# Kernel optimization log

Measured on AMD Instinct MI355X. Metric: run time of the kernel, lower is better.

The kernel has to match this reference:

```python
import jax, jax.numpy as jnp
from jax import lax
import numpy as np

NB_CODE = 16384
DIM = 128
SCALES = [(1, 1), (2, 2), (4, 4), (8, 8), (16, 16)]
PHI_IDX = [0, 1, 1, 2, 3]  # PhiPartiallyShared: argmin(|ticks - si/(SN-1)|), K=4, SN=5
RESI = 0.5  # abs(quant_resi)
BETA = 0.25


def _cubic(x, a=-0.75):
    # PyTorch bicubic kernel (cubic convolution, a=-0.75)
    ax = np.abs(x)
    return np.where(ax <= 1.0, (a + 2.0) * ax ** 3 - (a + 3.0) * ax ** 2 + 1.0,
                    np.where(ax < 2.0, a * ax ** 3 - 5.0 * a * ax ** 2 + 8.0 * a * ax - 4.0 * a, 0.0))


def bicubic_mat(n_in, n_out):
    # 1D interpolation matrix matching torch F.interpolate(mode='bicubic', align_corners=False)
    W = np.zeros((n_out, n_in), dtype=np.float32)
    scale = n_in / n_out
    for i in range(n_out):
        x = (i + 0.5) * scale - 0.5
        x0 = int(np.floor(x))
        t = x - x0
        for k in range(4):
            idx = min(max(x0 - 1 + k, 0), n_in - 1)  # border clamp
            W[i, idx] += _cubic(t + 1.0 - k)
    return jnp.asarray(W)


def phi_apply(h, w, b):
    y = lax.conv_general_dilated(h, w, (1, 1), 'SAME',
                                 dimension_numbers=('NCHW', 'OIHW', 'NCHW'))
    y = y + b[None, :, None, None]
    return h * (1.0 - RESI) + y * RESI


def setup_inputs() -> dict:
    key = jax.random.key(0)
    k1, k2, k3, k4 = jax.random.split(key, 4)
    B, C, J, L = 16, DIM, 16, 16
    f_bcjl = jax.random.normal(k1, (B, C, J, L), dtype=jnp.float32)
    emb = jax.random.normal(k2, (NB_CODE, C), dtype=jnp.float32) * 0.02
    # 4 partially-shared Phi convs (3x3, C->C)
    phi_w = jax.random.normal(k3, (4, C, C, 3, 3), dtype=jnp.float32) * (1.0 / np.sqrt(C * 9))
    phi_b = jax.random.normal(k4, (4, C), dtype=jnp.float32) * 0.01
    return {'f_bcjl': f_bcjl, 'emb': emb, 'phi_w': phi_w, 'phi_b': phi_b}


def reference(f_bcjl, emb, phi_w, phi_b):
    B, C, J, L = f_bcjl.shape
    SN = len(SCALES)
    f_ng = lax.stop_gradient(f_bcjl)
    f_rest = f_ng
    f_hat = jnp.zeros_like(f_ng)
    loss = jnp.float32(0.0)
    e_sq = jnp.sum(emb * emb, axis=1)  # [K]
    idx_all = []
    for si, (sn, tn) in enumerate(SCALES):
        if si != SN - 1:
            # 'area' downsample == integer-factor average pooling here
            r = f_rest.reshape(B, C, sn, J // sn, tn, L // tn).mean(axis=(3, 5))
        else:
            r = f_rest
        rNC = r.transpose(0, 2, 3, 1).reshape(-1, C)  # [N, C]
        d = jnp.sum(rNC * rNC, axis=1, keepdims=True) + e_sq - 2.0 * (rNC @ emb.T)
        idx = jnp.argmin(d, axis=1)  # [N]
        idx_all.append(idx)
        h = emb[idx].reshape(B, sn, tn, C).transpose(0, 3, 1, 2)  # [B,C,sn,tn]
        if si != SN - 1:
            Wj = bicubic_mat(sn, J)
            Wl = bicubic_mat(tn, L)
            h = jnp.einsum('js,bcst,lt->bcjl', Wj, h, Wl)
        k = PHI_IDX[si]
        h = phi_apply(h, phi_w[k], phi_b[k])
        f_hat = f_hat + h
        f_rest = f_rest - h
        loss = loss + BETA * jnp.mean((lax.stop_gradient(f_hat) - f_bcjl) ** 2) \
                    + jnp.mean((f_hat - f_ng) ** 2)
    loss = loss / SN
    idx_cat = jnp.concatenate(idx_all)
    counts = jnp.zeros((NB_CODE,), jnp.float32).at[idx_cat].add(1.0)
    p = counts / idx_cat.shape[0]
    perplexity = jnp.exp(-jnp.sum(p * jnp.log(p + 1e-10)))
    # straight-through estimator
    f_hat_out = lax.stop_gradient(f_hat) - f_ng + f_bcjl
    return (f_hat_out, loss, perplexity)
```

## Files before the change

kernel.cpp:

```cpp
#include <hip/hip_runtime.h>
#include <hip/hip_bf16.h>
#include <math.h>

#define BATCH 16
#define CDIM  128
#define NCODE 16384
#define ELEMS 524288
#define NTOT  5456
#define WEXT_TOT 589824
#define LOSS_COEF 4.76837158203125e-7f

typedef __attribute__((ext_vector_type(8))) short short8;
typedef __attribute__((ext_vector_type(4))) float float4v;
typedef unsigned short ushortT;
typedef unsigned long long u64;
typedef unsigned int u32;

__device__ __forceinline__ ushortT f2bf(float x) {
    __hip_bfloat16 h = __float2bfloat16(x);
    return *reinterpret_cast<ushortT*>(&h);
}
__device__ __forceinline__ float bf2f(ushortT b) {
    __hip_bfloat16 h = *reinterpret_cast<__hip_bfloat16*>(&b);
    return __bfloat162float(h);
}
__device__ __forceinline__ u32 ford(float v) {
    u32 b = __float_as_uint(v);
    return b ^ ((u32)((int)b >> 31) | 0x80000000u);
}

__device__ double cubic_d(double x) {
    const double a = -0.75;
    double ax = fabs(x);
    if (ax <= 1.0) return (a + 2.0) * ax * ax * ax - (a + 3.0) * ax * ax + 1.0;
    if (ax < 2.0)  return a * ax * ax * ax - 5.0 * a * ax * ax + 8.0 * a * ax - 4.0 * a;
    return 0.0;
}

__global__ __launch_bounds__(256)
void k_prologue(const float* __restrict__ f, const float* __restrict__ emb,
                const float* __restrict__ phi_w,
                float* __restrict__ f_rest, float* __restrict__ f_hat,
                float* __restrict__ esq, ushortT* __restrict__ embext,
                ushortT* __restrict__ wext, float* __restrict__ wmat,
                float* __restrict__ lossA) {
    const int t = threadIdx.x;
    const int id = blockIdx.x * 256 + t;

    if (id < ELEMS) {
        f_rest[id] = f[id];
        f_hat[id] = 0.f;
        int row = id >> 5, c4 = id & 31;
        float4 v = reinterpret_cast<const float4*>(emb + (size_t)row * CDIM)[c4];
        float xs[4] = {v.x, v.y, v.z, v.w};
        ushortT hi[4], lo[4];
        float ss = 0.f;
        #pragma unroll
        for (int i = 0; i < 4; ++i) {
            hi[i] = f2bf(xs[i]);
            lo[i] = f2bf(xs[i] - bf2f(hi[i]));
            ss += xs[i] * xs[i];
        }
        ushortT* base = embext + (size_t)row * 256;
        *reinterpret_cast<ushort4*>(base + c4 * 4)       = make_ushort4(hi[0], hi[1], hi[2], hi[3]);
        *reinterpret_cast<ushort4*>(base + 128 + c4 * 4) = make_ushort4(lo[0], lo[1], lo[2], lo[3]);
        #pragma unroll
        for (int off = 16; off; off >>= 1) ss += __shfl_down(ss, off);
        if ((t & 31) == 0) esq[row] = ss;
    }
    if (id < WEXT_TOT) {
        int k4 = id / 147456, rem = id % 147456;
        int co = rem / 1152, kk = rem % 1152;
        int off = kk >> 7, ci = kk & 127;
        float v = 0.5f * phi_w[(((size_t)(k4 * 128 + co)) * 128 + ci) * 9 + off];
        if (ci == co && off == 4) v += 0.5f;
        wext[id] = f2bf(v);
    }
    if (blockIdx.x == 0 && t < 64) {
        int sIdx = t >> 4;
        int S = 1 << sIdx;
        int j = t & 15;
        const int offs[4] = {0, 16, 48, 112};
        double row[8];
        for (int s = 0; s < 8; ++s) row[s] = 0.0;
        double scale = (double)S / 16.0;
        double x = (j + 0.5) * scale - 0.5;
        double x0 = floor(x);
        double tt = x - x0;
        for (int k = 0; k < 4; ++k) {
            int idx = (int)x0 - 1 + k;
            idx = idx < 0 ? 0 : (idx > S - 1 ? S - 1 : idx);
            row[idx] += cubic_d(tt + 1.0 - k);
        }
        for (int s = 0; s < S; ++s) wmat[offs[sIdx] + j * S + s] = (float)row[s];
    }
    if (id == 0) lossA[0] = 0.f;
}

__global__ __launch_bounds__(256)
void k_packext(const float* __restrict__ fr, ushortT* __restrict__ re,
               u64* __restrict__ packed, int N, int padN, int S, int lgS) {
    int id = blockIdx.x * 256 + threadIdx.x;
    if (id < N) packed[id] = ~0ull;
    if (id >= padN * 32) return;
    int row = id >> 5, c4 = id & 31;
    ushortT hi[4], lo[4];
    if (row < N) {
        int mask = S - 1;
        int tt = row & mask, ssi = (row >> lgS) & mask, b = row >> (2 * lgS);
        int bs = 16 >> lgS;
        float inv = 1.f / (float)(bs * bs);
        #pragma unroll
        for (int u = 0; u < 4; ++u) {
            int c = c4 * 4 + u;
            const float* base = fr + (size_t)(b * 128 + c) * 256 + (ssi * bs) * 16 + tt * bs;
            float acc = 0.f;
            for (int jj = 0; jj < bs; ++jj)
                for (int ll = 0; ll < bs; ++ll)
                    acc += base[jj * 16 + ll];
            float x = acc * inv;
            hi[u] = f2bf(x);
            lo[u] = f2bf(x - bf2f(hi[u]));
        }
    } else {
        #pragma unroll
        for (int u = 0; u < 4; ++u) { hi[u] = 0; lo[u] = 0; }
    }
    ushortT* base = re + (size_t)row * 256;
    *reinterpret_cast<ushort4*>(base + c4 * 4)       = make_ushort4(hi[0], hi[1], hi[2], hi[3]);
    *reinterpret_cast<ushort4*>(base + 128 + c4 * 4) = make_ushort4(lo[0], lo[1], lo[2], lo[3]);
}

__global__ __launch_bounds__(256)
void k_packext_wave(const float* __restrict__ fr, ushortT* __restrict__ re,
                    u64* __restrict__ packed, int N, int padN, int S, int lgS) {
    int gid = blockIdx.x * 256 + threadIdx.x;
    int wid = gid >> 6, lane = threadIdx.x & 63;
    if (wid >= padN * 128) return;
    int row = wid >> 7, c = wid & 127;
    float x = 0.f;
    if (row < N) {
        int mask = S - 1;
        int tt = row & mask, ssi = (row >> lgS) & mask, b = row >> (2 * lgS);
        int lgbs = 4 - lgS, bs = 1 << lgbs, cnt = bs * bs;
        const float* base = fr + (size_t)(b * 128 + c) * 256 + (ssi * bs) * 16 + tt * bs;
        float acc = 0.f;
        for (int e = lane; e < cnt; e += 64)
            acc += base[(e >> lgbs) * 16 + (e & (bs - 1))];
        #pragma unroll
        for (int off = 32; off; off >>= 1) acc += __shfl_down(acc, off);
        x = acc / (float)cnt;
    }
    if (lane == 0) {
        ushortT h = f2bf(x);
        re[(size_t)row * 256 + c] = h;
        re[(size_t)row * 256 + 128 + c] = f2bf(x - bf2f(h));
        if (c == 0 && row < N) packed[row] = ~0ull;
    }
}

template<int TI>
__global__ __launch_bounds__(256)
void k_argmin_mfma(const ushortT* __restrict__ rext, const ushortT* __restrict__ embext,
                   const float* __restrict__ esq, int N, int kPerSplit,
                   u64* __restrict__ packed) {
    __shared__ ushortT Btile[2][64 * 32 * 8];
    const int t = threadIdx.x;
    const int w = t >> 6;
    const int lane = t & 63;
    const int ln = lane & 15;
    const int q  = lane >> 4;
    const int k0beg = blockIdx.y * kPerSplit;
    const int rowW = blockIdx.x * (64 * TI) + w * (16 * TI);

    short8 a[TI][8];
    #pragma unroll
    for (int ti = 0; ti < TI; ++ti) {
        const ushortT* r0 = rext + (size_t)(rowW + ti * 16 + ln) * 256 + q * 8;
        #pragma unroll
        for (int sb = 0; sb < 8; ++sb)
            a[ti][sb] = *reinterpret_cast<const short8*>(r0 + sb * 32);
    }

    float minv[TI][4];
    int   mini[TI][4];
    #pragma unroll
    for (int ti = 0; ti < TI; ++ti)
        #pragma unroll
        for (int rg = 0; rg < 4; ++rg) { minv[ti][rg] = 3.4e38f; mini[ti][rg] = 0; }

    const int tiles = kPerSplit >> 6;

    #pragma unroll
    for (int i = 0; i < 8; ++i) {
        int F = (i * 4 + w) * 64 + lane;
        int n = F >> 5, cs = F & 31;
        int cp = (cs & ~7) | ((cs & 7) ^ (n & 7));
        const ushortT* src = embext + (size_t)(k0beg + n) * 256 + cp * 8;
        __builtin_amdgcn_global_load_lds(
            (const __attribute__((address_space(1))) unsigned int*)src,
            (__attribute__((address_space(3))) unsigned int*)&Btile[0][(size_t)((i * 4 + w) * 64) * 8],
            16, 0, 0);
    }

    for (int it = 0; it < tiles; ++it) {
        __syncthreads();
        if (it + 1 < tiles) {
            int k1 = k0beg + (it + 1) * 64;
            int bu = (it + 1) & 1;
            #pragma unroll
            for (int i = 0; i < 8; ++i) {
                int F = (i * 4 + w) * 64 + lane;
                int n = F >> 5, cs = F & 31;
                int cp = (cs & ~7) | ((cs & 7) ^ (n & 7));
                const ushortT* src = embext + (size_t)(k1 + n) * 256 + cp * 8;
                __builtin_amdgcn_global_load_lds(
                    (const __attribute__((address_space(1))) unsigned int*)src,
                    (__attribute__((address_space(3))) unsigned int*)&Btile[bu][(size_t)((i * 4 + w) * 64) * 8],
                    16, 0, 0);
            }
        }
        const ushortT* Bt = Btile[it & 1];
        const int k0 = k0beg + it * 64;

        #pragma unroll
        for (int sub = 0; sub < 4; ++sub) {
            int n = sub * 16 + ln;
            short8 bfr[8];
            #pragma unroll
            for (int sb = 0; sb < 8; ++sb) {
                int cp = q + 4 * sb;
                int cs = (cp & ~7) | ((cp & 7) ^ (n & 7));
                bfr[sb] = *reinterpret_cast<const short8*>(&Bt[(size_t)(n * 32 + cs) * 8]);
            }
            float4v acc[TI];
            #pragma unroll
            for (int ti = 0; ti < TI; ++ti) acc[ti] = (float4v){0.f, 0.f, 0.f, 0.f};
            #pragma unroll
            for (int s = 0; s < 12; ++s) {
                int as = s < 8 ? s : s - 8;
                int bs = s < 4 ? s : s - 4;
                #pragma unroll
                for (int ti = 0; ti < TI; ++ti)
                    acc[ti] = __builtin_amdgcn_mfma_f32_16x16x32_bf16(a[ti][as], bfr[bs], acc[ti], 0, 0, 0);
            }
            int kc = k0 + sub * 16 + ln;
            float es = esq[kc];
            #pragma unroll
            for (int ti = 0; ti < TI; ++ti)
                #pragma unroll
                for (int rg = 0; rg < 4; ++rg) {
                    float sc = fmaf(-2.f, acc[ti][rg], es);
                    if (sc < minv[ti][rg]) { minv[ti][rg] = sc; mini[ti][rg] = kc; }
                }
        }
    }

    #pragma unroll
    for (int ti = 0; ti < TI; ++ti)
        #pragma unroll
        for (int rg = 0; rg < 4; ++rg) {
            float v = minv[ti][rg]; int ix = mini[ti][rg];
            #pragma unroll
            for (int off = 1; off < 16; off <<= 1) {
                float ov = __shfl_xor(v, off);
                int   oi = __shfl_xor(ix, off);
                if (ov < v || (ov == v && oi < ix)) { v = ov; ix = oi; }
            }
            if (ln == 0) {
                int row = rowW + ti * 16 + q * 4 + rg;
                if (row < N) {
                    u64 p = ((u64)ford(v) << 32) | (u32)ix;
                    atomicMin(&packed[row], p);
                }
            }
        }
}

__global__ __launch_bounds__(256)
void k_upconv(const float* __restrict__ emb, const u64* __restrict__ packed,
              const float* __restrict__ wm, int S, int lastScale,
              const ushortT* __restrict__ wext, const float* __restrict__ bias,
              const float* __restrict__ f_in, float* __restrict__ f_hat,
              float* __restrict__ f_rest, float* __restrict__ loss_acc) {
    __shared__ __align__(16) ushortT Htile[3 * 16 * 128];
    __shared__ float wsum[4];
    const int t = threadIdx.x;
    const int b = blockIdx.x >> 4;
    const int j = blockIdx.x & 15;

    {
        const int l = t >> 4, c8 = t & 15;
        const int phys = (c8 & 8) | ((c8 & 7) ^ (l & 7));
        #pragma unroll
        for (int r = 0; r < 3; ++r) {
            int jin = j - 1 + r;
            float acc[8] = {0.f, 0.f, 0.f, 0.f, 0.f, 0.f, 0.f, 0.f};
            if (jin >= 0 && jin < 16) {
                if (lastScale) {
                    int idx = (int)(u32)(packed[(b * 16 + jin) * 16 + l] & 0xFFFFFFFFull);
                    const float* er = emb + (size_t)idx * CDIM + c8 * 8;
                    float4 e0 = *reinterpret_cast<const float4*>(er);
                    float4 e1 = *reinterpret_cast<const float4*>(er + 4);
                    acc[0] = e0.x; acc[1] = e0.y; acc[2] = e0.z; acc[3] = e0.w;
                    acc[4] = e1.x; acc[5] = e1.y; acc[6] = e1.z; acc[7] = e1.w;
                } else {
                    for (int s = 0; s < S; ++s) {
                        float wjv = wm[jin * S + s];
                        for (int tt2 = 0; tt2 < S; ++tt2) {
                            float wv = wjv * wm[l * S + tt2];
                            int idx = (int)(u32)(packed[b * S * S + s * S + tt2] & 0xFFFFFFFFull);
                            const float* er = emb + (size_t)idx * CDIM + c8 * 8;
                            float4 e0 = *reinterpret_cast<const float4*>(er);
                            float4 e1 = *reinterpret_cast<const float4*>(er + 4);
                            acc[0] += wv * e0.x; acc[1] += wv * e0.y;
                            acc[2] += wv * e0.z; acc[3] += wv * e0.w;
                            acc[4] += wv * e1.x; acc[5] += wv * e1.y;
                            acc[6] += wv * e1.z; acc[7] += wv * e1.w;
                        }
                    }
                }
            }
            short8 o;
            #pragma unroll
            for (int i = 0; i < 8; ++i) o[i] = (short)f2bf(acc[i]);
            *reinterpret_cast<short8*>(&Htile[((size_t)(r * 16 + l) * 16 + phys) * 8]) = o;
        }
    }
    __syncthreads();

    const int w = t >> 6, lane = t & 63;
    const int ln = lane & 15, q = lane >> 4;
    const int co0 = w * 32;
    const ushortT* wA = wext + (size_t)(co0 + ln) * 1152;
    float4v acc2[2] = {{0.f, 0.f, 0.f, 0.f}, {0.f, 0.f, 0.f, 0.f}};
    const short8 zz = {0, 0, 0, 0, 0, 0, 0, 0};

    #pragma unroll 3
    for (int off = 0; off < 9; ++off) {
        const int dj = off / 3, dl = off % 3;
        int cIn = ln + dl - 1;
        int cCl = cIn < 0 ? 0 : (cIn > 15 ? 15 : cIn);
        bool oob = (cIn != cCl);
        int rb = (dj * 16 + cCl) * 128;
        #pragma unroll
        for (int g = 0; g < 4; ++g) {
            int csl = g * 4 + q;
            int phys = (csl & 8) | ((csl & 7) ^ (cCl & 7));
            short8 av = *reinterpret_cast<const short8*>(&Htile[rb + phys * 8]);
            if (oob) av = zz;
            const ushortT* wr = wA + (off * 4 + g) * 32 + q * 8;
            short8 b0 = *reinterpret_cast<const short8*>(wr);
            short8 b1 = *reinterpret_cast<const short8*>(wr + 16 * 1152);
            acc2[0] = __builtin_amdgcn_mfma_f32_16x16x32_bf16(av, b0, acc2[0], 0, 0, 0);
            acc2[1] = __builtin_amdgcn_mfma_f32_16x16x32_bf16(av, b1, acc2[1], 0, 0, 0);
        }
    }

    float s = 0.f;
    #pragma unroll
    for (int sn = 0; sn < 2; ++sn) {
        int co = co0 + sn * 16 + ln;
        float bsv = 0.5f * bias[co];
        size_t gi = ((size_t)(b * 128 + co) * 16 + j) * 16 + q * 4;
        float4 fh = *reinterpret_cast<const float4*>(&f_hat[gi]);
        float4 fr = *reinterpret_cast<const float4*>(&f_rest[gi]);
        float4 fv = *reinterpret_cast<const float4*>(&f_in[gi]);
        float o0 = acc2[sn][0] + bsv, o1 = acc2[sn][1] + bsv;
        float o2 = acc2[sn][2] + bsv, o3 = acc2[sn][3] + bsv;
        fh.x += o0; fh.y += o1; fh.z += o2; fh.w += o3;
        fr.x -= o0; fr.y -= o1; fr.z -= o2; fr.w -= o3;
        *reinterpret_cast<float4*>(&f_hat[gi]) = fh;
        *reinterpret_cast<float4*>(&f_rest[gi]) = fr;
        float d0 = fh.x - fv.x, d1 = fh.y - fv.y;
        float d2 = fh.z - fv.z, d3 = fh.w - fv.w;
        s += d0 * d0 + d1 * d1 + d2 * d2 + d3 * d3;
    }
    #pragma unroll
    for (int off = 32; off; off >>= 1) s += __shfl_down(s, off);
    if (lane == 0) wsum[w] = s;
    __syncthreads();
    if (t == 0)
        atomicAdd(loss_acc, (wsum[0] + wsum[1] + wsum[2] + wsum[3]) * LOSS_COEF);
}

__global__ __launch_bounds__(256)
void k_final(const u64* __restrict__ packed, const float* __restrict__ loss_acc,
             float* __restrict__ out) {
    __shared__ u32 cnt2[NCODE / 2];
    __shared__ float ws4[4];
    int t = threadIdx.x;
    for (int i = t; i < NCODE / 2; i += 256) cnt2[i] = 0;
    __syncthreads();
    for (int i = t; i < NTOT; i += 256) {
        int idx = (int)(u32)(packed[i] & 0xFFFFFFFFull);
        atomicAdd(&cnt2[idx >> 1], (idx & 1) ? 65536u : 1u);
    }
    __syncthreads();
    float s = 0.f;
    for (int k = t; k < NCODE; k += 256) {
        u32 c = cnt2[k >> 1];
        c = (k & 1) ? (c >> 16) : (c & 0xFFFFu);
        float p = (float)c * (1.0f / (float)NTOT);
        s += p * logf(p + 1e-10f);
    }
    #pragma unroll
    for (int off = 32; off; off >>= 1) s += __shfl_down(s, off);
    if ((t & 63) == 0) ws4[t >> 6] = s;
    __syncthreads();
    if (t == 0) {
        out[ELEMS]     = loss_acc[0];
        out[ELEMS + 1] = expf(-(ws4[0] + ws4[1] + ws4[2] + ws4[3]));
    }
}

extern "C" void kernel_launch(void* const* d_in, const int* in_sizes, int n_in,
                              void* d_out, int out_size, void* d_ws, size_t ws_size,
                              hipStream_t stream) {
    const float* f     = (const float*)d_in[0];
    const float* emb   = (const float*)d_in[1];
    const float* phi_w = (const float*)d_in[2];
    const float* phi_b = (const float*)d_in[3];
    float* out = (float*)d_out;

    float* wsf = (float*)d_ws;
    float*   f_rest = wsf;
    float*   esq    = wsf + 524288;
    float*   wmat   = wsf + 540672;
    float*   lossA  = wsf + 540928;
    u64*     packed = (u64*)(wsf + 540992);
    ushortT* embext = (ushortT*)(wsf + 557376);
    ushortT* rext   = (ushortT*)(wsf + 2654528);
    ushortT* wext   = (ushortT*)(wsf + 3178816);

    k_prologue<<<2304, 256, 0, stream>>>(f, emb, phi_w, f_rest, out, esq,
                                         embext, wext, wmat, lossA);

    const int Ss[5]     = {1, 2, 4, 8, 16};
    const int lgSs[5]   = {0, 1, 2, 3, 4};
    const int phiIdx[5] = {0, 1, 1, 2, 3};
    const int ksplit[5] = {256, 256, 256, 64, 16};
    const int TIa[5]    = {2, 2, 4, 4, 4};
    const int wmOff[5]  = {0, 16, 48, 112, 0};
    const int pOff[5]   = {0, 16, 80, 336, 1360};

    for (int si = 0; si < 5; ++si) {
        int S = Ss[si], lgS = lgSs[si];
        int N = 16 * S * S;
        int TI = TIa[si];
        int align = 64 * TI;
        int padN = (N + align - 1) & ~(align - 1);
        u64* pk = packed + pOff[si];

        if (S <= 2)
            k_packext_wave<<<padN * 128 / 4, 256, 0, stream>>>(f_rest, rext, pk, N, padN, S, lgS);
        else
            k_packext<<<padN * 32 / 256, 256, 0, stream>>>(f_rest, rext, pk, N, padN, S, lgS);

        int KS = ksplit[si];
        if (TI == 2)
            k_argmin_mfma<2><<<dim3(padN / 128, KS), 256, 0, stream>>>(rext, embext, esq,
                                                                       N, NCODE / KS, pk);
        else
            k_argmin_mfma<4><<<dim3(padN / 256, KS), 256, 0, stream>>>(rext, embext, esq,
                                                                       N, NCODE / KS, pk);

        int k = phiIdx[si];
        k_upconv<<<256, 256, 0, stream>>>(emb, pk, wmat + wmOff[si], S, si == 4 ? 1 : 0,
                                          wext + (size_t)k * 147456,
                                          phi_b + (size_t)k * 128, f, out, f_rest, lossA);
    }

    k_final<<<1, 256, 0, stream>>>(packed, lossA, out);
}
```

Before: 384.3 us.

## Separate bicubic upsample into two passes via shared memory; retune split and tile sizes

```diff
diff --git a/kernel.cpp b/kernel.cpp
--- a/kernel.cpp
+++ b/kernel.cpp
@@ -284,42 +284,70 @@
               const float* __restrict__ f_in, float* __restrict__ f_hat,
               float* __restrict__ f_rest, float* __restrict__ loss_acc) {
     __shared__ __align__(16) ushortT Htile[3 * 16 * 128];
+    __shared__ __align__(16) float tmpS[3 * 8 * 128];
     __shared__ float wsum[4];
     const int t = threadIdx.x;
     const int b = blockIdx.x >> 4;
     const int j = blockIdx.x & 15;
-
-    {
-        const int l = t >> 4, c8 = t & 15;
-        const int phys = (c8 & 8) | ((c8 & 7) ^ (l & 7));
+    const int l = t >> 4, c8 = t & 15;
+    const int phys = (c8 & 8) | ((c8 & 7) ^ (l & 7));
+
+    if (lastScale) {
         #pragma unroll
         for (int r = 0; r < 3; ++r) {
             int jin = j - 1 + r;
             float acc[8] = {0.f, 0.f, 0.f, 0.f, 0.f, 0.f, 0.f, 0.f};
             if (jin >= 0 && jin < 16) {
-                if (lastScale) {
-                    int idx = (int)(u32)(packed[(b * 16 + jin) * 16 + l] & 0xFFFFFFFFull);
-                    const float* er = emb + (size_t)idx * CDIM + c8 * 8;
+                int idx = (int)(u32)(packed[(b * 16 + jin) * 16 + l] & 0xFFFFFFFFull);
+                const float* er = emb + (size_t)idx * CDIM + c8 * 8;
+                float4 e0 = *reinterpret_cast<const float4*>(er);
+                float4 e1 = *reinterpret_cast<const float4*>(er + 4);
+                acc[0] = e0.x; acc[1] = e0.y; acc[2] = e0.z; acc[3] = e0.w;
+                acc[4] = e1.x; acc[5] = e1.y; acc[6] = e1.z; acc[7] = e1.w;
+            }
+            short8 o;
+            #pragma unroll
+            for (int i = 0; i < 8; ++i) o[i] = (short)f2bf(acc[i]);
+            *reinterpret_cast<short8*>(&Htile[((size_t)(r * 16 + l) * 16 + phys) * 8]) = o;
+        }
+    } else {
+        int items = 3 * S * 16;
+        for (int i = t; i < items; i += 256) {
+            int r = i / (S * 16);
+            int rem = i - r * (S * 16);
+            int t2 = rem >> 4, cc8 = rem & 15;
+            int jin = j - 1 + r;
+            float a0[8] = {0.f, 0.f, 0.f, 0.f, 0.f, 0.f, 0.f, 0.f};
+            if (jin >= 0 && jin < 16) {
+                for (int s = 0; s < S; ++s) {
+                    float wjv = wm[jin * S + s];
+                    int idx = (int)(u32)(packed[b * S * S + s * S + t2] & 0xFFFFFFFFull);
+                    const float* er = emb + (size_t)idx * CDIM + cc8 * 8;
                     float4 e0 = *reinterpret_cast<const float4*>(er);
                     float4 e1 = *reinterpret_cast<const float4*>(er + 4);
-                    acc[0] = e0.x; acc[1] = e0.y; acc[2] = e0.z; acc[3] = e0.w;
-                    acc[4] = e1.x; acc[5] = e1.y; acc[6] = e1.z; acc[7] = e1.w;
-                } else {
-                    for (int s = 0; s < S; ++s) {
-                        float wjv = wm[jin * S + s];
-                        for (int tt2 = 0; tt2 < S; ++tt2) {
-                            float wv = wjv * wm[l * S + tt2];
-                            int idx = (int)(u32)(packed[b * S * S + s * S + tt2] & 0xFFFFFFFFull);
-                            const float* er = emb + (size_t)idx * CDIM + c8 * 8;
-                            float4 e0 = *reinterpret_cast<const float4*>(er);
-                            float4 e1 = *reinterpret_cast<const float4*>(er + 4);
-                            acc[0] += wv * e0.x; acc[1] += wv * e0.y;
-                            acc[2] += wv * e0.z; acc[3] += wv * e0.w;
-                            acc[4] += wv * e1.x; acc[5] += wv * e1.y;
-                            acc[6] += wv * e1.z; acc[7] += wv * e1.w;
-                        }
-                    }
+                    a0[0] += wjv * e0.x; a0[1] += wjv * e0.y;
+                    a0[2] += wjv * e0.z; a0[3] += wjv * e0.w;
+                    a0[4] += wjv * e1.x; a0[5] += wjv * e1.y;
+                    a0[6] += wjv * e1.z; a0[7] += wjv * e1.w;
                 }
+            }
+            float* tp = &tmpS[((size_t)(r * 8 + t2)) * 128 + cc8 * 8];
+            *reinterpret_cast<float4*>(tp)     = make_float4(a0[0], a0[1], a0[2], a0[3]);
+            *reinterpret_cast<float4*>(tp + 4) = make_float4(a0[4], a0[5], a0[6], a0[7]);
+        }
+        __syncthreads();
+        #pragma unroll
+        for (int r = 0; r < 3; ++r) {
+            float acc[8] = {0.f, 0.f, 0.f, 0.f, 0.f, 0.f, 0.f, 0.f};
+            for (int t2 = 0; t2 < S; ++t2) {
+                float wlv = wm[l * S + t2];
+                const float* tp = &tmpS[((size_t)(r * 8 + t2)) * 128 + c8 * 8];
+                float4 v0 = *reinterpret_cast<const float4*>(tp);
+                float4 v1 = *reinterpret_cast<const float4*>(tp + 4);
+                acc[0] += wlv * v0.x; acc[1] += wlv * v0.y;
+                acc[2] += wlv * v0.z; acc[3] += wlv * v0.w;
+                acc[4] += wlv * v1.x; acc[5] += wlv * v1.y;
+                acc[6] += wlv * v1.z; acc[7] += wlv * v1.w;
             }
             short8 o;
             #pragma unroll
@@ -346,8 +374,8 @@
         #pragma unroll
         for (int g = 0; g < 4; ++g) {
             int csl = g * 4 + q;
-            int phys = (csl & 8) | ((csl & 7) ^ (cCl & 7));
-            short8 av = *reinterpret_cast<const short8*>(&Htile[rb + phys * 8]);
+            int ph2 = (csl & 8) | ((csl & 7) ^ (cCl & 7));
+            short8 av = *reinterpret_cast<const short8*>(&Htile[rb + ph2 * 8]);
             if (oob) av = zz;
             const ushortT* wr = wA + (off * 4 + g) * 32 + q * 8;
             short8 b0 = *reinterpret_cast<const short8*>(wr);
@@ -439,8 +467,8 @@
     const int Ss[5]     = {1, 2, 4, 8, 16};
     const int lgSs[5]   = {0, 1, 2, 3, 4};
     const int phiIdx[5] = {0, 1, 1, 2, 3};
-    const int ksplit[5] = {256, 256, 256, 64, 16};
-    const int TIa[5]    = {2, 2, 4, 4, 4};
+    const int ksplit[5] = {256, 256, 128, 64, 32};
+    const int TIa[5]    = {2, 2, 2, 2, 4};
     const int wmOff[5]  = {0, 16, 48, 112, 0};
     const int pOff[5]   = {0, 16, 80, 336, 1360};
 
```

Measured after the change: 341.6 us. 11.1% less time.
